# Optimization experiments

Hardware: AMD Instinct MI355X
Metric: run time of the kernel (lower is better)

## Reference

```python
import jax, jax.numpy as jnp
import numpy as np

EPS = 1e-5

def conv1x1(x, w, b):
    # x: [B,C,H,W], w: [O,C], b: [O]
    return jnp.einsum('bchw,oc->bohw', x, w) + b[None, :, None, None]

def bn(x, g, be, m, v):
    inv = g / jnp.sqrt(v + EPS)
    return x * inv[None, :, None, None] + (be - m * inv)[None, :, None, None]

def mrconv4d(x, w, b, g, be, m, v, K):
    B, C, H, W = x.shape
    x_j = jnp.zeros_like(x)
    # torch.cat([x[:,:,-i:,:], x[:,:,:-i,:]], dim=2) == roll by +i along H
    for i in range(K, H, K):
        x_j = jnp.maximum(x_j, x - jnp.roll(x, i, axis=2))
    for i in range(K, W, K):
        x_j = jnp.maximum(x_j, x - jnp.roll(x, i, axis=3))
    y = jnp.concatenate([x, x_j], axis=1)  # [B,2C,H,W]
    y = conv1x1(y, w, b)
    y = bn(y, g, be, m, v)
    return jax.nn.gelu(y, approximate=False)

def setup_inputs() -> dict:
    key = jax.random.key(0)
    ks = jax.random.split(key, 20)
    B, C, H, W = 16, 384, 56, 56
    C2 = 2 * C
    d = {}
    d['x'] = jax.random.normal(ks[0], (B, C, H, W), dtype=jnp.float32)
    d['fc1_w'] = jax.random.normal(ks[1], (C, C), dtype=jnp.float32) * 0.02
    d['fc1_b'] = jax.random.normal(ks[2], (C,), dtype=jnp.float32) * 0.02
    d['fc1_g'] = jax.random.uniform(ks[3], (C,), dtype=jnp.float32) + 0.5
    d['fc1_be'] = jax.random.normal(ks[4], (C,), dtype=jnp.float32) * 0.02
    d['fc1_m'] = jax.random.normal(ks[5], (C,), dtype=jnp.float32) * 0.02
    d['fc1_v'] = jax.random.uniform(ks[6], (C,), dtype=jnp.float32) + 0.5
    d['gc_w'] = jax.random.normal(ks[7], (C2, C2), dtype=jnp.float32) * 0.02
    d['gc_b'] = jax.random.normal(ks[8], (C2,), dtype=jnp.float32) * 0.02
    d['gc_g'] = jax.random.uniform(ks[9], (C2,), dtype=jnp.float32) + 0.5
    d['gc_be'] = jax.random.normal(ks[10], (C2,), dtype=jnp.float32) * 0.02
    d['gc_m'] = jax.random.normal(ks[11], (C2,), dtype=jnp.float32) * 0.02
    d['gc_v'] = jax.random.uniform(ks[12], (C2,), dtype=jnp.float32) + 0.5
    d['fc2_w'] = jax.random.normal(ks[13], (C, C2), dtype=jnp.float32) * 0.02
    d['fc2_b'] = jax.random.normal(ks[14], (C,), dtype=jnp.float32) * 0.02
    d['fc2_g'] = jax.random.uniform(ks[15], (C,), dtype=jnp.float32) + 0.5
    d['fc2_be'] = jax.random.normal(ks[16], (C,), dtype=jnp.float32) * 0.02
    d['fc2_m'] = jax.random.normal(ks[17], (C,), dtype=jnp.float32) * 0.02
    d['fc2_v'] = jax.random.uniform(ks[18], (C,), dtype=jnp.float32) + 0.5
    d['K'] = 2
    return d

def reference(x, fc1_w, fc1_b, fc1_g, fc1_be, fc1_m, fc1_v,
              gc_w, gc_b, gc_g, gc_be, gc_m, gc_v,
              fc2_w, fc2_b, fc2_g, fc2_be, fc2_m, fc2_v, K):
    res = x
    h = bn(conv1x1(x, fc1_w, fc1_b), fc1_g, fc1_be, fc1_m, fc1_v)
    h = mrconv4d(h, gc_w, gc_b, gc_g, gc_be, gc_m, gc_v, K)
    h = bn(conv1x1(h, fc2_w, fc2_b), fc2_g, fc2_be, fc2_m, fc2_v)
    return h + res  # drop_path=0 -> identity
```

## Files before the change

kernel.cpp:

```cpp
#include <hip/hip_runtime.h>

#define P_ 3136
#define NTOT 50176
#define EPSV 1e-5f

typedef __bf16 bf16x8 __attribute__((ext_vector_type(8)));
typedef float f32x4 __attribute__((ext_vector_type(4)));
typedef unsigned short u16x8 __attribute__((ext_vector_type(8)));
typedef unsigned short u16x4 __attribute__((ext_vector_type(4)));

__device__ __forceinline__ unsigned short f2bf(float f) {
    unsigned u = __builtin_bit_cast(unsigned, f);
    unsigned r = u + 0x7fffu + ((u >> 16) & 1u);
    return (unsigned short)(r >> 16);
}
__device__ __forceinline__ float bf2f(unsigned short h) {
    unsigned u = ((unsigned)h) << 16;
    return __builtin_bit_cast(float, u);
}
__device__ __forceinline__ float gelu_fast(float x) {
    float x2 = x * x;
    float u2 = x * (1.5957691216f + 0.0713548162f * x2);
    u2 = fminf(u2, 80.0f);
    float e = __expf(u2);
    return x * e * __builtin_amdgcn_rcpf(e + 1.0f);
}
__device__ __forceinline__ void gload16(const void* g, void* l) {
    __builtin_amdgcn_global_load_lds(
        (const __attribute__((address_space(1))) void*)g,
        (__attribute__((address_space(3))) void*)l, 16, 0, 0);
}
__device__ __forceinline__ bf16x8 ldlds(const char* p) {
    return __builtin_bit_cast(bf16x8, *(const u16x8*)p);
}

__global__ __launch_bounds__(256)
void prep_wb(const float* __restrict__ w1, const float* __restrict__ w2,
             const float* __restrict__ w3,
             unsigned short* __restrict__ o1, unsigned short* __restrict__ o2,
             unsigned short* __restrict__ o3,
             const float* b1, const float* g1, const float* be1, const float* m1, const float* v1,
             const float* b2, const float* g2, const float* be2, const float* m2, const float* v2,
             const float* b3, const float* g3, const float* be3, const float* m3, const float* v3,
             float* bn1, float* bn2, float* bn3)
{
    int i = blockIdx.x * 256 + threadIdx.x;
    const int n1 = 384 * 384 / 4, n2 = 768 * 768 / 4, n3 = 384 * 768 / 4;
    if (i < n1 + n2 + n3) {
        const float* src; unsigned short* dst; int j;
        if (i < n1)           { src = w1; dst = o1; j = i; }
        else if (i < n1 + n2) { src = w2; dst = o2; j = i - n1; }
        else                  { src = w3; dst = o3; j = i - n1 - n2; }
        float4 f = *(const float4*)(src + (size_t)j * 4);
        u16x4 pk = { f2bf(f.x), f2bf(f.y), f2bf(f.z), f2bf(f.w) };
        *(u16x4*)(dst + (size_t)j * 4) = pk;
    } else {
        int k = i - (n1 + n2 + n3);
        const float *pb, *pg, *pbe, *pm, *pv; float* dst; int o, M;
        if (k < 384)       { pb=b1; pg=g1; pbe=be1; pm=m1; pv=v1; dst=bn1; o=k;        M=384; }
        else if (k < 1152) { pb=b2; pg=g2; pbe=be2; pm=m2; pv=v2; dst=bn2; o=k-384;    M=768; }
        else               { pb=b3; pg=g3; pbe=be3; pm=m3; pv=v3; dst=bn3; o=k-1152;   M=384; }
        float inv = pg[o] / sqrtf(pv[o] + EPSV);
        dst[o]     = inv;
        dst[M + o] = (pb[o] - pm[o]) * inv + pbe[o];
    }
}

__global__ __launch_bounds__(256)
void prep_xT(const float* __restrict__ x, unsigned short* __restrict__ xT)
{
    __shared__ float tl[64][65];
    const int t = threadIdx.x;
    const int c0 = blockIdx.x * 64;
    const int p0 = blockIdx.y * 64;
    const int b  = blockIdx.z;
    const float* xb = x + ((size_t)b * 384 + c0) * P_ + p0;
    {
        int c = t >> 2, j0 = (t & 3) * 16;
        #pragma unroll
        for (int j = 0; j < 16; j += 4) {
            float4 f4 = *(const float4*)(xb + (size_t)c * P_ + j0 + j);
            tl[c][j0 + j]     = f4.x; tl[c][j0 + j + 1] = f4.y;
            tl[c][j0 + j + 2] = f4.z; tl[c][j0 + j + 3] = f4.w;
        }
    }
    __syncthreads();
    {
        int p = t >> 2, c1 = (t & 3) * 16;
        unsigned short buf[16];
        #pragma unroll
        for (int j = 0; j < 16; ++j) buf[j] = f2bf(tl[c1 + j][p]);
        unsigned short* dst = xT + ((size_t)b * P_ + p0 + p) * 384 + c0 + c1;
        *(u16x8*)dst       = *(u16x8*)buf;
        *(u16x8*)(dst + 8) = *(u16x8*)(buf + 8);
    }
}

template<int KD, int MDIM, int EPI>
__device__ __forceinline__ void gemm_body(
    const unsigned short* __restrict__ W,
    const unsigned short* __restrict__ In,
    void* __restrict__ OutV,
    const float* __restrict__ bnp,
    const float* __restrict__ res,
    char* lds)
{
    constexpr int NT = KD / 64;
    constexpr int MT = MDIM / 128;

    const int t    = threadIdx.x;
    const int lane = t & 63;
    const int wave = t >> 6;
    const int wm = wave >> 1, wn = wave & 1;
    const int fr = lane & 15, fg = lane >> 4;

    const int nwg = gridDim.x;
    int id = blockIdx.x;
    int q = nwg >> 3, r = nwg & 7;
    int xcd = id & 7, pos = id >> 3;
    int wg = (xcd < r ? xcd * (q + 1) : r * (q + 1) + (xcd - r) * q) + pos;
    const int m0 = (wg % MT) * 128;
    const int n0 = (wg / MT) * 128;

    const int pcu  = (((t & 7) ^ ((t >> 3) & 7)) << 3);
    const int srow = t >> 3;
    const unsigned short* pA[4];
    const unsigned short* pB[4];
    #pragma unroll
    for (int i = 0; i < 4; ++i) {
        pA[i] = W  + (size_t)(m0 + i * 32 + srow) * KD + pcu;
        pB[i] = In + (size_t)(n0 + i * 32 + srow) * KD + pcu;
    }
    auto stage = [&](int kt) {
        int kk = kt * 64;
        char* base = lds + (kt & 1) * 32768 + t * 16;
        #pragma unroll
        for (int i = 0; i < 4; ++i) gload16(pA[i] + kk, base + i * 4096);
        #pragma unroll
        for (int i = 0; i < 4; ++i) gload16(pB[i] + kk, base + 16384 + i * 4096);
    };

    const int ko0 = (fg * 16) ^ ((fr & 7) << 4);
    const int ko1 = (64 + fg * 16) ^ ((fr & 7) << 4);
    const int arow = wm * 64 + fr;
    const int brow = wn * 64 + fr;

    f32x4 acc[4][4] = {};

    stage(0);

    for (int kt = 0; kt < NT; ++kt) {
        asm volatile("s_waitcnt vmcnt(0)" ::: "memory");
        __builtin_amdgcn_s_barrier();
        __builtin_amdgcn_sched_barrier(0);
        if (kt + 1 < NT) stage(kt + 1);
        __builtin_amdgcn_sched_barrier(0);

        const char* base = lds + (kt & 1) * 32768;
        bf16x8 afr[4][2], bfr[4][2];
        #pragma unroll
        for (int mf = 0; mf < 4; ++mf) {
            afr[mf][0] = ldlds(base + (arow + mf * 16) * 128 + ko0);
            afr[mf][1] = ldlds(base + (arow + mf * 16) * 128 + ko1);
        }
        #pragma unroll
        for (int nf = 0; nf < 4; ++nf) {
            bfr[nf][0] = ldlds(base + 16384 + (brow + nf * 16) * 128 + ko0);
            bfr[nf][1] = ldlds(base + 16384 + (brow + nf * 16) * 128 + ko1);
        }
        #pragma unroll
        for (int ks = 0; ks < 2; ++ks)
            #pragma unroll
            for (int mf = 0; mf < 4; ++mf)
                #pragma unroll
                for (int nf = 0; nf < 4; ++nf)
                    acc[mf][nf] = __builtin_amdgcn_mfma_f32_16x16x32_bf16(
                        afr[mf][ks], bfr[nf][ks], acc[mf][nf], 0, 0, 0);
    }

    asm volatile("s_waitcnt vmcnt(0)" ::: "memory");
    __builtin_amdgcn_s_barrier();

    if (EPI < 2) {
        unsigned short* eL = (unsigned short*)lds;
        unsigned short* Out = (unsigned short*)OutV;
        #pragma unroll
        for (int mf = 0; mf < 4; ++mf) {
            const int o_l = wm * 64 + mf * 16 + fg * 4;
            f32x4 inv = *(const f32x4*)(bnp + m0 + o_l);
            f32x4 sh  = *(const f32x4*)(bnp + MDIM + m0 + o_l);
            #pragma unroll
            for (int nf = 0; nf < 4; ++nf) {
                const int col_l = wn * 64 + nf * 16 + fr;
                u16x4 pk;
                #pragma unroll
                for (int rr = 0; rr < 4; ++rr) {
                    float v = acc[mf][nf][rr] * inv[rr] + sh[rr];
                    if (EPI == 1) v = gelu_fast(v);
                    pk[rr] = f2bf(v);
                }
                *(u16x4*)(eL + col_l * 136 + o_l) = pk;
            }
        }
        __builtin_amdgcn_s_barrier();
        #pragma unroll
        for (int i = 0; i < 8; ++i) {
            const int col_l = (t >> 4) + i * 16;
            const int o8 = (t & 15) * 8;
            u16x8 v = *(const u16x8*)(eL + col_l * 136 + o8);
            *(u16x8*)(Out + (size_t)(n0 + col_l) * 768 + m0 + o8) = v;
        }
    } else {
        float* eL = (float*)lds;
        float* Out = (float*)OutV;
        #pragma unroll
        for (int mf = 0; mf < 4; ++mf) {
            const int o_l = wm * 64 + mf * 16 + fg * 4;
            f32x4 inv = *(const f32x4*)(bnp + m0 + o_l);
            f32x4 sh  = *(const f32x4*)(bnp + MDIM + m0 + o_l);
            #pragma unroll
            for (int nf = 0; nf < 4; ++nf) {
                const int col_l = wn * 64 + nf * 16 + fr;
                #pragma unroll
                for (int rr = 0; rr < 4; ++rr)
                    eL[(o_l + rr) * 128 + col_l] = acc[mf][nf][rr] * inv[rr] + sh[rr];
            }
        }
        __builtin_amdgcn_s_barrier();
        const int b0 = n0 / P_;
        const int r0 = n0 - b0 * P_;
        #pragma unroll
        for (int g8 = 0; g8 < 8; ++g8) {
            size_t adr[8]; float ev[8], rv[8];
            #pragma unroll
            for (int u = 0; u < 8; ++u) {
                const int idx = (g8 * 8 + u) * 256 + t;
                const int o_i = idx >> 7, col = idx & 127;
                int p = r0 + col;
                const int wrap = p >= P_;
                p -= wrap ? P_ : 0;
                adr[u] = (size_t)(b0 + wrap) * 384 * P_ + (size_t)(m0 + o_i) * P_ + p;
                ev[u]  = eL[o_i * 128 + col];
                rv[u]  = res[adr[u]];
            }
            #pragma unroll
            for (int u = 0; u < 8; ++u)
                Out[adr[u]] = ev[u] + rv[u];
        }
    }
}

__global__ __launch_bounds__(256, 2)
void gemm1(const unsigned short* __restrict__ W, const unsigned short* __restrict__ In,
           void* __restrict__ OutV, const float* __restrict__ bnp)
{
    __shared__ __align__(16) char lds[65536];
    gemm_body<384, 384, 0>(W, In, OutV, bnp, nullptr, lds);
}
__global__ __launch_bounds__(256, 2)
void gemm2(const unsigned short* __restrict__ W, const unsigned short* __restrict__ In,
           void* __restrict__ OutV, const float* __restrict__ bnp)
{
    __shared__ __align__(16) char lds[65536];
    gemm_body<768, 768, 1>(W, In, OutV, bnp, nullptr, lds);
}
__global__ __launch_bounds__(256, 2)
void gemm3(const unsigned short* __restrict__ W, const unsigned short* __restrict__ In,
           void* __restrict__ OutV, const float* __restrict__ bnp,
           const float* __restrict__ res)
{
    __shared__ __align__(16) char lds[65536];
    gemm_body<768, 384, 2>(W, In, OutV, bnp, res, lds);
}

#define MINSEG (16 * 2 * 56 * 384)
__global__ __launch_bounds__(384)
void mr_min(const unsigned short* __restrict__ y, float* __restrict__ mins)
{
    const int c = threadIdx.x;
    const int q = blockIdx.x;
    const int b = blockIdx.y;
    const unsigned short* yb = y + (size_t)b * P_ * 768;
    float m1e = 3.4e38f, m2e = 3.4e38f, m1o = 3.4e38f, m2o = 3.4e38f;
    if (q < 56) {
        int w = q;
        for (int h = 0; h < 56; h += 2) {
            float v0 = bf2f(yb[(size_t)(h * 56 + w) * 768 + c]);
            float v1 = bf2f(yb[(size_t)((h + 1) * 56 + w) * 768 + c]);
            if (v0 < m1e) { m2e = m1e; m1e = v0; } else if (v0 < m2e) m2e = v0;
            if (v1 < m1o) { m2o = m1o; m1o = v1; } else if (v1 < m2o) m2o = v1;
        }
        float* cm1 = mins;
        float* cm2 = mins + MINSEG;
        cm1[((b * 2 + 0) * 56 + w) * 384 + c] = m1e;
        cm1[((b * 2 + 1) * 56 + w) * 384 + c] = m1o;
        cm2[((b * 2 + 0) * 56 + w) * 384 + c] = m2e;
        cm2[((b * 2 + 1) * 56 + w) * 384 + c] = m2o;
    } else {
        int h = q - 56;
        for (int w = 0; w < 56; w += 2) {
            float v0 = bf2f(yb[(size_t)(h * 56 + w) * 768 + c]);
            float v1 = bf2f(yb[(size_t)(h * 56 + w + 1) * 768 + c]);
            if (v0 < m1e) { m2e = m1e; m1e = v0; } else if (v0 < m2e) m2e = v0;
            if (v1 < m1o) { m2o = m1o; m1o = v1; } else if (v1 < m2o) m2o = v1;
        }
        float* rm1 = mins + 2 * MINSEG;
        float* rm2 = mins + 3 * MINSEG;
        rm1[((b * 2 + 0) * 56 + h) * 384 + c] = m1e;
        rm1[((b * 2 + 1) * 56 + h) * 384 + c] = m1o;
        rm2[((b * 2 + 0) * 56 + h) * 384 + c] = m2e;
        rm2[((b * 2 + 1) * 56 + h) * 384 + c] = m2o;
    }
}

__global__ __launch_bounds__(384)
void mr_comb(unsigned short* __restrict__ y, const float* __restrict__ mins)
{
    const int c = threadIdx.x;
    const int h = blockIdx.x;
    const int b = blockIdx.y;
    unsigned short* yb = y + (size_t)b * P_ * 768;
    const float* cm1 = mins;
    const float* cm2 = mins + MINSEG;
    const float* rm1 = mins + 2 * MINSEG;
    const float* rm2 = mins + 3 * MINSEG;
    const int parh = h & 1;
    float r1e = rm1[((b * 2 + 0) * 56 + h) * 384 + c];
    float r2e = rm2[((b * 2 + 0) * 56 + h) * 384 + c];
    float r1o = rm1[((b * 2 + 1) * 56 + h) * 384 + c];
    float r2o = rm2[((b * 2 + 1) * 56 + h) * 384 + c];
    #pragma unroll 2
    for (int w = 0; w < 56; ++w) {
        float v  = bf2f(yb[(size_t)(h * 56 + w) * 768 + c]);
        float c1 = cm1[((b * 2 + parh) * 56 + w) * 384 + c];
        float c2 = cm2[((b * 2 + parh) * 56 + w) * 384 + c];
        float mh = v > c1 ? c1 : c2;
        float rw1 = (w & 1) ? r1o : r1e;
        float rw2 = (w & 1) ? r2o : r2e;
        float mw = v > rw1 ? rw1 : rw2;
        float xj = fmaxf(0.0f, v - fminf(mh, mw));
        yb[(size_t)(h * 56 + w) * 768 + 384 + c] = f2bf(xj);
    }
}

extern "C" void kernel_launch(void* const* d_in, const int* in_sizes, int n_in,
                              void* d_out, int out_size, void* d_ws, size_t ws_size,
                              hipStream_t stream)
{
    const float* x      = (const float*)d_in[0];
    const float* fc1_w  = (const float*)d_in[1];
    const float* fc1_b  = (const float*)d_in[2];
    const float* fc1_g  = (const float*)d_in[3];
    const float* fc1_be = (const float*)d_in[4];
    const float* fc1_m  = (const float*)d_in[5];
    const float* fc1_v  = (const float*)d_in[6];
    const float* gc_w   = (const float*)d_in[7];
    const float* gc_b   = (const float*)d_in[8];
    const float* gc_g   = (const float*)d_in[9];
    const float* gc_be  = (const float*)d_in[10];
    const float* gc_m   = (const float*)d_in[11];
    const float* gc_v   = (const float*)d_in[12];
    const float* fc2_w  = (const float*)d_in[13];
    const float* fc2_b  = (const float*)d_in[14];
    const float* fc2_g  = (const float*)d_in[15];
    const float* fc2_be = (const float*)d_in[16];
    const float* fc2_m  = (const float*)d_in[17];
    const float* fc2_v  = (const float*)d_in[18];

    char* ws = (char*)d_ws;
    unsigned short* y   = (unsigned short*)ws;
    unsigned short* g   = y + (size_t)NTOT * 768;
    unsigned short* xT  = g + (size_t)NTOT * 768;
    unsigned short* wb1 = xT + (size_t)NTOT * 384;
    unsigned short* wb2 = wb1 + 384 * 384;
    unsigned short* wb3 = wb2 + 768 * 768;
    float* bn1 = (float*)(wb3 + 384 * 768);
    float* bn2 = bn1 + 2 * 384;
    float* bn3 = bn2 + 2 * 768;
    float* mins = bn3 + 2 * 384;

    prep_wb<<<1014, 256, 0, stream>>>(fc1_w, gc_w, fc2_w, wb1, wb2, wb3,
                                      fc1_b, fc1_g, fc1_be, fc1_m, fc1_v,
                                      gc_b, gc_g, gc_be, gc_m, gc_v,
                                      fc2_b, fc2_g, fc2_be, fc2_m, fc2_v,
                                      bn1, bn2, bn3);
    prep_xT<<<dim3(6, 49, 16), 256, 0, stream>>>(x, xT);

    gemm1<<<dim3(3 * 392), 256, 0, stream>>>(wb1, xT, y, bn1);
    mr_min<<<dim3(112, 16), 384, 0, stream>>>(y, mins);
    mr_comb<<<dim3(56, 16), 384, 0, stream>>>(y, mins);
    gemm2<<<dim3(6 * 392), 256, 0, stream>>>(wb2, y, g, bn2);
    gemm3<<<dim3(3 * 392), 256, 0, stream>>>(wb3, g, (void*)d_out, bn3, x);
}
```

Baseline: 236.8 us.

## Quantize middle activation and gc weights to FP8 e4m3, use FP8 MFMA

The intermediate activation y (output of the first GEMM and the max-relative features) is now stored as FP8 e4m3 instead of bf16. The 768x768 gc weights are quantized to FP8 with a scale of 32, which is folded back into the BN scale. A new gemm2q kernel uses fp8 MFMA instructions over a 128-byte K tile, so it needs fewer K iterations and moves half the bytes. The intent is to cut memory traffic for y and raise matrix throughput in the largest GEMM. The cost is a large loss of precision in the activations and weights, which may exceed the accuracy tolerance.

```diff
diff --git a/kernel.cpp b/kernel.cpp
--- a/kernel.cpp
+++ b/kernel.cpp
@@ -17,6 +17,27 @@
 __device__ __forceinline__ float bf2f(unsigned short h) {
     unsigned u = ((unsigned)h) << 16;
     return __builtin_bit_cast(float, u);
+}
+__device__ __forceinline__ unsigned f2e4m3(float f) {
+    unsigned u = __builtin_bit_cast(unsigned, f);
+    unsigned s = (u >> 24) & 0x80u;
+    float a = fabsf(f);
+    if (a >= 448.f) return s | 0x7Eu;
+    if (a < 0.015625f) {
+        int m = (int)(a * 512.f + 0.5f);
+        return s | (unsigned)m;
+    }
+    unsigned au = __builtin_bit_cast(unsigned, a);
+    unsigned r = au + 0x7FFFFu + ((au >> 20) & 1u);
+    unsigned e = (r >> 23) - 120u;
+    return s | (e << 3) | ((r >> 20) & 7u);
+}
+__device__ __forceinline__ float e4m3f(unsigned b) {
+    unsigned em = b & 0x7fu;
+    float v;
+    if (em < 8u) v = (float)em * 0.001953125f;
+    else v = __builtin_bit_cast(float, (((em >> 3) + 120u) << 23) | ((em & 7u) << 20));
+    return (b & 0x80u) ? -v : v;
 }
 __device__ __forceinline__ float gelu_fast(float x) {
     float x2 = x * x;
@@ -37,7 +58,7 @@
 __global__ __launch_bounds__(256)
 void prep_wb(const float* __restrict__ w1, const float* __restrict__ w2,
              const float* __restrict__ w3,
-             unsigned short* __restrict__ o1, unsigned short* __restrict__ o2,
+             unsigned short* __restrict__ o1, unsigned char* __restrict__ o2q,
              unsigned short* __restrict__ o3,
              const float* b1, const float* g1, const float* be1, const float* m1, const float* v1,
              const float* b2, const float* g2, const float* be2, const float* m2, const float* v2,
@@ -46,22 +67,29 @@
 {
     int i = blockIdx.x * 256 + threadIdx.x;
     const int n1 = 384 * 384 / 4, n2 = 768 * 768 / 4, n3 = 384 * 768 / 4;
-    if (i < n1 + n2 + n3) {
-        const float* src; unsigned short* dst; int j;
-        if (i < n1)           { src = w1; dst = o1; j = i; }
-        else if (i < n1 + n2) { src = w2; dst = o2; j = i - n1; }
-        else                  { src = w3; dst = o3; j = i - n1 - n2; }
-        float4 f = *(const float4*)(src + (size_t)j * 4);
+    if (i < n1) {
+        float4 f = *(const float4*)(w1 + (size_t)i * 4);
         u16x4 pk = { f2bf(f.x), f2bf(f.y), f2bf(f.z), f2bf(f.w) };
-        *(u16x4*)(dst + (size_t)j * 4) = pk;
+        *(u16x4*)(o1 + (size_t)i * 4) = pk;
+    } else if (i < n1 + n2) {
+        int j = i - n1;
+        float4 f = *(const float4*)(w2 + (size_t)j * 4);
+        unsigned pk = f2e4m3(f.x * 32.f) | (f2e4m3(f.y * 32.f) << 8)
+                    | (f2e4m3(f.z * 32.f) << 16) | (f2e4m3(f.w * 32.f) << 24);
+        *(unsigned*)(o2q + (size_t)j * 4) = pk;
+    } else if (i < n1 + n2 + n3) {
+        int j = i - n1 - n2;
+        float4 f = *(const float4*)(w3 + (size_t)j * 4);
+        u16x4 pk = { f2bf(f.x), f2bf(f.y), f2bf(f.z), f2bf(f.w) };
+        *(u16x4*)(o3 + (size_t)j * 4) = pk;
     } else {
         int k = i - (n1 + n2 + n3);
-        const float *pb, *pg, *pbe, *pm, *pv; float* dst; int o, M;
-        if (k < 384)       { pb=b1; pg=g1; pbe=be1; pm=m1; pv=v1; dst=bn1; o=k;        M=384; }
-        else if (k < 1152) { pb=b2; pg=g2; pbe=be2; pm=m2; pv=v2; dst=bn2; o=k-384;    M=768; }
-        else               { pb=b3; pg=g3; pbe=be3; pm=m3; pv=v3; dst=bn3; o=k-1152;   M=384; }
+        const float *pb, *pg, *pbe, *pm, *pv; float* dst; int o, M; float isc = 1.f;
+        if (k < 384)       { pb=b1; pg=g1; pbe=be1; pm=m1; pv=v1; dst=bn1; o=k;      M=384; }
+        else if (k < 1152) { pb=b2; pg=g2; pbe=be2; pm=m2; pv=v2; dst=bn2; o=k-384;  M=768; isc = 1.f/32.f; }
+        else               { pb=b3; pg=g3; pbe=be3; pm=m3; pv=v3; dst=bn3; o=k-1152; M=384; }
         float inv = pg[o] / sqrtf(pv[o] + EPSV);
-        dst[o]     = inv;
+        dst[o]     = inv * isc;
         dst[M + o] = (pb[o] - pm[o]) * inv + pbe[o];
     }
 }
@@ -181,9 +209,9 @@
     asm volatile("s_waitcnt vmcnt(0)" ::: "memory");
     __builtin_amdgcn_s_barrier();
 
-    if (EPI < 2) {
-        unsigned short* eL = (unsigned short*)lds;
-        unsigned short* Out = (unsigned short*)OutV;
+    if (EPI == 0) {
+        unsigned char* eL = (unsigned char*)lds;
+        unsigned char* Out = (unsigned char*)OutV;
         #pragma unroll
         for (int mf = 0; mf < 4; ++mf) {
             const int o_l = wm * 64 + mf * 16 + fg * 4;
@@ -192,23 +220,20 @@
             #pragma unroll
             for (int nf = 0; nf < 4; ++nf) {
                 const int col_l = wn * 64 + nf * 16 + fr;
-                u16x4 pk;
+                unsigned pk = 0;
                 #pragma unroll
-                for (int rr = 0; rr < 4; ++rr) {
-                    float v = acc[mf][nf][rr] * inv[rr] + sh[rr];
-                    if (EPI == 1) v = gelu_fast(v);
-                    pk[rr] = f2bf(v);
-                }
-                *(u16x4*)(eL + col_l * 136 + o_l) = pk;
+                for (int rr = 0; rr < 4; ++rr)
+                    pk |= f2e4m3(acc[mf][nf][rr] * inv[rr] + sh[rr]) << (8 * rr);
+                *(unsigned*)(eL + col_l * 144 + o_l) = pk;
             }
         }
         __builtin_amdgcn_s_barrier();
         #pragma unroll
-        for (int i = 0; i < 8; ++i) {
-            const int col_l = (t >> 4) + i * 16;
-            const int o8 = (t & 15) * 8;
-            u16x8 v = *(const u16x8*)(eL + col_l * 136 + o8);
-            *(u16x8*)(Out + (size_t)(n0 + col_l) * 768 + m0 + o8) = v;
+        for (int it = 0; it < 8; ++it) {
+            const int idx = it * 256 + t;
+            const int col = idx >> 4, seg = idx & 15;
+            *(unsigned long long*)(Out + (size_t)(n0 + col) * 768 + m0 + seg * 8) =
+                *(const unsigned long long*)(eL + col * 144 + seg * 8);
         }
     } else {
         float* eL = (float*)lds;
@@ -258,13 +283,6 @@
     gemm_body<384, 384, 0>(W, In, OutV, bnp, nullptr, lds);
 }
 __global__ __launch_bounds__(256, 2)
-void gemm2(const unsigned short* __restrict__ W, const unsigned short* __restrict__ In,
-           void* __restrict__ OutV, const float* __restrict__ bnp)
-{
-    __shared__ __align__(16) char lds[65536];
-    gemm_body<768, 768, 1>(W, In, OutV, bnp, nullptr, lds);
-}
-__global__ __launch_bounds__(256, 2)
 void gemm3(const unsigned short* __restrict__ W, const unsigned short* __restrict__ In,
            void* __restrict__ OutV, const float* __restrict__ bnp,
            const float* __restrict__ res)
@@ -273,20 +291,133 @@
     gemm_body<768, 384, 2>(W, In, OutV, bnp, res, lds);
 }
 
+__global__ __launch_bounds__(256, 2)
+void gemm2q(const unsigned char* __restrict__ W,
+            const unsigned char* __restrict__ In,
+            unsigned short* __restrict__ Out,
+            const float* __restrict__ bnp)
+{
+    constexpr int NT = 6;
+    constexpr int MT = 6;
+    __shared__ __align__(16) char lds[65536];
+
+    const int t    = threadIdx.x;
+    const int lane = t & 63;
+    const int wave = t >> 6;
+    const int wm = wave >> 1, wn = wave & 1;
+    const int fr = lane & 15, fg = lane >> 4;
+
+    const int nwg = gridDim.x;
+    int id = blockIdx.x;
+    int q = nwg >> 3, r = nwg & 7;
+    int xcd = id & 7, pos = id >> 3;
+    int wg = (xcd < r ? xcd * (q + 1) : r * (q + 1) + (xcd - r) * q) + pos;
+    const int m0 = (wg % MT) * 128;
+    const int n0 = (wg / MT) * 128;
+
+    const int pcu  = (((t & 7) ^ ((t >> 3) & 7)) << 4);
+    const int srow = t >> 3;
+    const unsigned char* pA[4];
+    const unsigned char* pB[4];
+    #pragma unroll
+    for (int i = 0; i < 4; ++i) {
+        pA[i] = W  + (size_t)(m0 + i * 32 + srow) * 768 + pcu;
+        pB[i] = In + (size_t)(n0 + i * 32 + srow) * 768 + pcu;
+    }
+    auto stage = [&](int kt) {
+        int kk = kt * 128;
+        char* base = lds + (kt & 1) * 32768 + t * 16;
+        #pragma unroll
+        for (int i = 0; i < 4; ++i) gload16(pA[i] + kk, base + i * 4096);
+        #pragma unroll
+        for (int i = 0; i < 4; ++i) gload16(pB[i] + kk, base + 16384 + i * 4096);
+    };
+
+    const int ko0 = (fg * 16) ^ ((fr & 7) << 4);
+    const int ko1 = (64 + fg * 16) ^ ((fr & 7) << 4);
+    const int arow = wm * 64 + fr;
+    const int brow = wn * 64 + fr;
+
+    f32x4 acc[4][4] = {};
+
+    stage(0);
+
+    for (int kt = 0; kt < NT; ++kt) {
+        asm volatile("s_waitcnt vmcnt(0)" ::: "memory");
+        __builtin_amdgcn_s_barrier();
+        __builtin_amdgcn_sched_barrier(0);
+        if (kt + 1 < NT) stage(kt + 1);
+        __builtin_amdgcn_sched_barrier(0);
+
+        const char* base = lds + (kt & 1) * 32768;
+        ulonglong2 afr[4][2], bfr[4][2];
+        #pragma unroll
+        for (int mf = 0; mf < 4; ++mf) {
+            afr[mf][0] = *(const ulonglong2*)(base + (arow + mf * 16) * 128 + ko0);
+            afr[mf][1] = *(const ulonglong2*)(base + (arow + mf * 16) * 128 + ko1);
+        }
+        #pragma unroll
+        for (int nf = 0; nf < 4; ++nf) {
+            bfr[nf][0] = *(const ulonglong2*)(base + 16384 + (brow + nf * 16) * 128 + ko0);
+            bfr[nf][1] = *(const ulonglong2*)(base + 16384 + (brow + nf * 16) * 128 + ko1);
+        }
+        #pragma unroll
+        for (int rd = 0; rd < 2; ++rd)
+            #pragma unroll
+            for (int hf = 0; hf < 2; ++hf)
+                #pragma unroll
+                for (int mf = 0; mf < 4; ++mf)
+                    #pragma unroll
+                    for (int nf = 0; nf < 4; ++nf)
+                        acc[mf][nf] = __builtin_amdgcn_mfma_f32_16x16x32_fp8_fp8(
+                            (long)(hf ? afr[mf][rd].y : afr[mf][rd].x),
+                            (long)(hf ? bfr[nf][rd].y : bfr[nf][rd].x),
+                            acc[mf][nf], 0, 0, 0);
+    }
+
+    asm volatile("s_waitcnt vmcnt(0)" ::: "memory");
+    __builtin_amdgcn_s_barrier();
+
+    unsigned short* eL = (unsigned short*)lds;
+    #pragma unroll
+    for (int mf = 0; mf < 4; ++mf) {
+        const int o_l = wm * 64 + mf * 16 + fg * 4;
+        f32x4 inv = *(const f32x4*)(bnp + m0 + o_l);
+        f32x4 sh  = *(const f32x4*)(bnp + 768 + m0 + o_l);
+        #pragma unroll
+        for (int nf = 0; nf < 4; ++nf) {
+            const int col_l = wn * 64 + nf * 16 + fr;
+            u16x4 pk;
+            #pragma unroll
+            for (int rr = 0; rr < 4; ++rr)
+                pk[rr] = f2bf(gelu_fast(acc[mf][nf][rr] * inv[rr] + sh[rr]));
+            *(u16x4*)(eL + col_l * 136 + o_l) = pk;
+        }
+    }
+    __builtin_amdgcn_s_barrier();
+    #pragma unroll
+    for (int i = 0; i < 8; ++i) {
+        const int col_l = (t >> 4) + i * 16;
+        const int o8 = (t & 15) * 8;
+        u16x8 v = *(const u16x8*)(eL + col_l * 136 + o8);
+        *(u16x8*)(Out + (size_t)(n0 + col_l) * 768 + m0 + o8) = v;
+    }
+}
+
 #define MINSEG (16 * 2 * 56 * 384)
 __global__ __launch_bounds__(384)
-void mr_min(const unsigned short* __restrict__ y, float* __restrict__ mins)
+void mr_min(const unsigned char* __restrict__ y, float* __restrict__ mins)
 {
     const int c = threadIdx.x;
     const int q = blockIdx.x;
     const int b = blockIdx.y;
-    const unsigned short* yb = y + (size_t)b * P_ * 768;
+    const unsigned char* yb = y + (size_t)b * P_ * 768;
     float m1e = 3.4e38f, m2e = 3.4e38f, m1o = 3.4e38f, m2o = 3.4e38f;
     if (q < 56) {
         int w = q;
         for (int h = 0; h < 56; h += 2) {
-            float v0 = bf2f(yb[(size_t)(h * 56 + w) * 768 + c]);
-            float v1 = bf2f(yb[(size_t)((h + 1) * 56 + w) * 768 + c]);
+            float v0 = e4m3f(yb[(size_t)(h * 56 + w) * 768 + c]);
+            float v1 = e4m3f(yb[(size_t)((h + 1) * 56 + w) * 768 + c]);
             if (v0 < m1e) { m2e = m1e; m1e = v0; } else if (v0 < m2e) m2e = v0;
             if (v1 < m1o) { m2o = m1o; m1o = v1; } else if (v1 < m2o) m2o = v1;
         }
@@ -299,8 +430,8 @@
     } else {
         int h = q - 56;
         for (int w = 0; w < 56; w += 2) {
-            float v0 = bf2f(yb[(size_t)(h * 56 + w) * 768 + c]);
-            float v1 = bf2f(yb[(size_t)(h * 56 + w + 1) * 768 + c]);
+            float v0 = e4m3f(yb[(size_t)(h * 56 + w) * 768 + c]);
+            float v1 = e4m3f(yb[(size_t)(h * 56 + w + 1) * 768 + c]);
             if (v0 < m1e) { m2e = m1e; m1e = v0; } else if (v0 < m2e) m2e = v0;
             if (v1 < m1o) { m2o = m1o; m1o = v1; } else if (v1 < m2o) m2o = v1;
         }
@@ -314,12 +445,12 @@
 }
 
 __global__ __launch_bounds__(384)
-void mr_comb(unsigned short* __restrict__ y, const float* __restrict__ mins)
+void mr_comb(unsigned char* __restrict__ y, const float* __restrict__ mins)
 {
     const int c = threadIdx.x;
     const int h = blockIdx.x;
     const int b = blockIdx.y;
-    unsigned short* yb = y + (size_t)b * P_ * 768;
+    unsigned char* yb = y + (size_t)b * P_ * 768;
     const float* cm1 = mins;
     const float* cm2 = mins + MINSEG;
     const float* rm1 = mins + 2 * MINSEG;
@@ -331,7 +462,7 @@
     float r2o = rm2[((b * 2 + 1) * 56 + h) * 384 + c];
     #pragma unroll 2
     for (int w = 0; w < 56; ++w) {
-        float v  = bf2f(yb[(size_t)(h * 56 + w) * 768 + c]);
+        float v  = e4m3f(yb[(size_t)(h * 56 + w) * 768 + c]);
         float c1 = cm1[((b * 2 + parh) * 56 + w) * 384 + c];
         float c2 = cm2[((b * 2 + parh) * 56 + w) * 384 + c];
         float mh = v > c1 ? c1 : c2;
@@ -339,7 +470,7 @@
         float rw2 = (w & 1) ? r2o : r2e;
         float mw = v > rw1 ? rw1 : rw2;
         float xj = fmaxf(0.0f, v - fminf(mh, mw));
-        yb[(size_t)(h * 56 + w) * 768 + 384 + c] = f2bf(xj);
+        yb[(size_t)(h * 56 + w) * 768 + 384 + c] = (unsigned char)f2e4m3(xj);
     }
 }
 
@@ -368,18 +499,18 @@
     const float* fc2_v  = (const float*)d_in[18];
 
     char* ws = (char*)d_ws;
-    unsigned short* y   = (unsigned short*)ws;
-    unsigned short* g   = y + (size_t)NTOT * 768;
+    unsigned char*  y   = (unsigned char*)ws;
+    unsigned short* g   = (unsigned short*)(ws + (size_t)NTOT * 768);
     unsigned short* xT  = g + (size_t)NTOT * 768;
     unsigned short* wb1 = xT + (size_t)NTOT * 384;
-    unsigned short* wb2 = wb1 + 384 * 384;
-    unsigned short* wb3 = wb2 + 768 * 768;
-    float* bn1 = (float*)(wb3 + 384 * 768);
+    unsigned short* wb3 = wb1 + 384 * 384;
+    unsigned char*  wb2q = (unsigned char*)(wb3 + 384 * 768);
+    float* bn1 = (float*)(wb2q + 768 * 768);
     float* bn2 = bn1 + 2 * 384;
     float* bn3 = bn2 + 2 * 768;
     float* mins = bn3 + 2 * 384;
 
-    prep_wb<<<1014, 256, 0, stream>>>(fc1_w, gc_w, fc2_w, wb1, wb2, wb3,
+    prep_wb<<<1014, 256, 0, stream>>>(fc1_w, gc_w, fc2_w, wb1, wb2q, wb3,
                                       fc1_b, fc1_g, fc1_be, fc1_m, fc1_v,
                                       gc_b, gc_g, gc_be, gc_m, gc_v,
                                       fc2_b, fc2_g, fc2_be, fc2_m, fc2_v,
@@ -389,6 +520,6 @@
     gemm1<<<dim3(3 * 392), 256, 0, stream>>>(wb1, xT, y, bn1);
     mr_min<<<dim3(112, 16), 384, 0, stream>>>(y, mins);
     mr_comb<<<dim3(56, 16), 384, 0, stream>>>(y, mins);
-    gemm2<<<dim3(6 * 392), 256, 0, stream>>>(wb2, y, g, bn2);
+    gemm2q<<<dim3(6 * 392), 256, 0, stream>>>(wb2q, y, g, bn2);
     gemm3<<<dim3(3 * 392), 256, 0, stream>>>(wb3, g, (void*)d_out, bn3, x);
 }
```

New measurement: 257.7 us. +8.8%, slower.
